# Optimization experiments

Hardware: AMD Instinct MI355X
Metric: run time of the kernel (lower is better)

Reference implementation:

```python
import jax, jax.numpy as jnp
import numpy as np

# Fixed architecture constants (match init_kwargs)
B, CIN, H, W = 2, 3, 224, 224
COUT = 64
KH = KW = 7
SH = SW = 2
PAD = 3
GROUPS = 1
MIX = 4
CG = COUT // GROUPS          # channels per group
REL = CG // 2                # rel_size
PH, PW = H + 2 * PAD, W + 2 * PAD          # padded spatial dims (230, 230)
FH = (PH - KH) // SH + 1                    # output height (112)
FW = (PW - KW) // SW + 1                    # output width  (112)


def setup_inputs() -> dict:
    key = jax.random.key(0)
    ks = jax.random.split(key, 10)
    n = jax.random.normal
    return {
        "x": n(ks[0], (B, CIN, H, W), jnp.float32),
        "weight_query": n(ks[1], (GROUPS, CIN // GROUPS, CG), jnp.float32) * 0.2,
        "weight_key": n(ks[2], (GROUPS, CIN // GROUPS, CG), jnp.float32) * 0.2,
        "weight_value": n(ks[3], (MIX, GROUPS, CIN // GROUPS, CG), jnp.float32) * 0.2,
        "relative_x": n(ks[4], (REL, 1, KW), jnp.float32) * 0.1,
        "relative_y": n(ks[5], (CG - REL, KH, 1), jnp.float32) * 0.1,
        "emb_x": n(ks[6], (CG, 1, PW), jnp.float32) * 0.1,
        "emb_y": n(ks[7], (CG, PH, 1), jnp.float32) * 0.1,
        "emb_m": n(ks[8], (MIX, CG, 1, 1), jnp.float32) * 0.1,
        "bias": n(ks[9], (COUT,), jnp.float32) * 0.05,
    }


def _unfold(t):
    """torch.nn.functional.unfold: (b,c,PH,PW) -> (b,c,KH*KW,FH*FW) with (c,kh,kw) layout."""
    b, c = t.shape[0], t.shape[1]
    ri = jnp.arange(FH) * SH
    rj = jnp.arange(FW) * SW
    p = t[:, :, ri[:, None] + jnp.arange(KH)[None, :], :]          # (b,c,FH,KH,PW)
    p = p[:, :, :, :, rj[:, None] + jnp.arange(KW)[None, :]]       # (b,c,FH,KH,FW,KW)
    return p.transpose(0, 1, 3, 5, 2, 4).reshape(b, c, KH * KW, FH * FW)


def _forward(x, wq, wk, wv, rx, ry, ex, ey, em, bias):
    b = x.shape[0]
    # relative position bias: (COUT, KH*KW, 1)
    rel = jnp.concatenate([jnp.tile(rx, (1, KH, 1)), jnp.tile(ry, (1, 1, KW))], axis=0)
    rel = jnp.tile(rel, (GROUPS, 1, 1)).reshape(COUT, KH * KW, 1)

    xp = jnp.pad(x, ((0, 0), (0, 0), (PAD, PAD), (PAD, PAD)))       # (b,CIN,PH,PW)
    x_ij = xp.transpose(0, 2, 3, 1).reshape(b, PH * PW, GROUPS, CIN // GROUPS)

    # per-pixel grouped projections -> (b, COUT, PH, PW)
    vq = jnp.einsum('bngi,gio->bgon', x_ij, wq).reshape(b, COUT, PH, PW)
    vk = jnp.einsum('bngi,gio->bgon', x_ij, wk).reshape(b, COUT, PH, PW)

    # mixture weights over value transforms: softmax over mix axis, per pixel
    p_ab = ex + ey                                                   # (CG,PH,PW)
    p_abm = jax.nn.softmax(jnp.sum(p_ab[None] * em, axis=1), axis=0) # (MIX,PH,PW)

    vvm = jnp.einsum('bngi,mgio->mbgon', x_ij, wv).reshape(MIX, b, COUT, PH, PW)
    vv = jnp.sum(vvm * p_abm[:, None, None], axis=0)                 # (b,COUT,PH,PW)

    win_k = _unfold(vk)                                              # (b,COUT,KH*KW,L)
    win_v = _unfold(vv)                                              # (b,COUT,KH*KW,L)
    # center query of each window (equivalent to unfold then slice center)
    ci = (KH - 1) // 2 + jnp.arange(FH) * SH
    cj = (KW - 1) // 2 + jnp.arange(FW) * SW
    win_q = vq[:, :, ci[:, None], cj[None, :]].reshape(b, COUT, 1, FH * FW)

    scores = jnp.sum(win_q * (win_k + rel[None]), axis=1)            # (b,KH*KW,L)
    # NOTE: the torch code applies softmax over dim=2 which, after the sum over
    # channels, is the SPATIAL dim (L), not the window dim. Faithful to source.
    attn = jax.nn.softmax(scores, axis=2)                            # (b,KH*KW,L)
    v = jnp.sum(attn[:, None] * win_v, axis=2) + bias[None, :, None] # (b,COUT,L)
    return v.reshape(b, COUT, FH, FW)


def reference(x, weight_query, weight_key, weight_value, relative_x, relative_y, emb_x, emb_y, emb_m, bias):
    return _forward(x, weight_query, weight_key, weight_value, relative_x, relative_y, emb_x, emb_y, emb_m, bias)
```

## Files before the change

### kernel.cpp

```cpp
#include <hip/hip_runtime.h>
#include <math.h>

namespace {
constexpr int Bc = 2, Hc = 224, Wc = 224, HWc = Hc * Wc;
constexpr int COUTc = 64, KHc = 7, KWc = 7, PADc = 3;
constexpr int MIXc = 4, RELc = 32;
constexpr int PHc = 230, PWc = 230;
constexpr int FHc = 112, FWc = 112, NN = FHc * FWc;
constexpr int NK = KHc * KWc;
constexpr int WS_EEX = 0;
constexpr int WS_EEY = WS_EEX + MIXc * PWc;
constexpr int WS_COL = WS_EEY + MIXc * PHc;
constexpr int WS_ACC = 1920;
}

__global__ __launch_bounds__(256) void sam_k0(
    const float* __restrict__ ex, const float* __restrict__ ey,
    const float* __restrict__ em, const float* __restrict__ wq,
    const float* __restrict__ wk, const float* __restrict__ rx,
    const float* __restrict__ ry, float* __restrict__ ws) {
  const int idx = blockIdx.x * 256 + threadIdx.x;
  if (idx < Bc * NK) ws[WS_ACC + idx * 16] = 0.f;

  constexpr int half = MIXc * PWc;
  if (idx < 2 * half) {
    const int which = idx >= half;
    const int r = which ? idx - half : idx;
    const int m = r / PWc, j = r % PWc;
    float s = 0.f;
#pragma unroll 8
    for (int c = 0; c < COUTc; ++c)
      s += (which ? ey[c * PHc + j] : ex[c * PWc + j]) * em[m * COUTc + c];
    ws[idx] = expf(s);
  }

  const int u = idx - 2 * half;
  if (u >= 0 && u < 51) {
    float s = 0.f;
    if (u < 9) {
      const int cj = u / 3, ci = u % 3;
#pragma unroll 8
      for (int o = 0; o < COUTc; ++o) s += wq[cj * COUTc + o] * wk[ci * COUTc + o];
    } else if (u < 30) {
      const int v = u - 9, cj = v / 7, kw = v % 7;
#pragma unroll 8
      for (int o = 0; o < RELc; ++o) s += wq[cj * COUTc + o] * rx[o * KWc + kw];
    } else {
      const int v = u - 30, cj = v / 7, kh = v % 7;
#pragma unroll 8
      for (int o = 0; o < RELc; ++o) s += wq[cj * COUTc + RELc + o] * ry[o * KHc + kh];
    }
    ws[WS_COL + u] = s;
  }
}

__global__ __launch_bounds__(256) void sam_stats(const float* __restrict__ x,
                                                 float* __restrict__ ws) {
  __shared__ float sCol[51];
  const int t = threadIdx.x;
  if (t < 51) sCol[t] = ws[WS_COL + t];
  __syncthreads();

  const int w = t >> 6, lane = t & 63;
  const int k = blockIdx.y * 4 + w;
  if (k >= NK) return;
  const int b = blockIdx.z;
  const int kh = k / 7, kw = k - 7 * kh;
  const int n = blockIdx.x * 64 + lane;
  const int fh = n / FWc, fw = n - fh * FWc;
  const int i0 = 2 * fh, j0 = 2 * fw;
  const float* xb = x + (size_t)b * 3 * HWc;
  const int co = i0 * Wc + j0;
  const float xc0 = xb[co], xc1 = xb[HWc + co], xc2 = xb[2 * HWc + co];
  const float* M = sCol;
  const float* Rx = sCol + 9;
  const float* Ry = sCol + 30;

  float s = xc0 * (Rx[kw] + Ry[kh]) + xc1 * (Rx[7 + kw] + Ry[7 + kh]) +
            xc2 * (Rx[14 + kw] + Ry[14 + kh]);
  const int ir = i0 + kh - PADc, jc = j0 + kw - PADc;
  if ((unsigned)ir < (unsigned)Hc && (unsigned)jc < (unsigned)Wc) {
    const float q0 = xc0 * M[0] + xc1 * M[3] + xc2 * M[6];
    const float q1 = xc0 * M[1] + xc1 * M[4] + xc2 * M[7];
    const float q2 = xc0 * M[2] + xc1 * M[5] + xc2 * M[8];
    const int off = ir * Wc + jc;
    s += q0 * xb[off] + q1 * xb[HWc + off] + q2 * xb[2 * HWc + off];
  }
  float e = expf(s);
#pragma unroll
  for (int m2 = 32; m2; m2 >>= 1) e += __shfl_xor(e, m2, 64);
  if (lane == 0) atomicAdd(ws + WS_ACC + ((size_t)b * NK + k) * 16, e);
}

__global__ __launch_bounds__(512) void sam_out(
    const float* __restrict__ x, const float* __restrict__ wv,
    const float* __restrict__ bias, const float* __restrict__ ws,
    float* __restrict__ out) {
  __shared__ float sCol[51];
  __shared__ float sdninv[NK];
  __shared__ float swv[12 * 64];
  __shared__ float sbias[64];
  __shared__ float sT[8][64][13];

  const int t = threadIdx.x;
  const int b = blockIdx.y;
  if (t < 51) sCol[t] = ws[WS_COL + t];
  if (t < NK) sdninv[t] = 1.f / ws[WS_ACC + ((size_t)b * NK + t) * 16];
  if (t < 64) sbias[t] = bias[t];
  for (int i = t; i < 12 * 64; i += 512) swv[i] = wv[i];
  __syncthreads();

  const int w = t >> 6, l = t & 63;
  const int n = blockIdx.x * 64 + l;
  const int fh = n / FWc, fw = n - fh * FWc;
  const int i0 = 2 * fh, j0 = 2 * fw;
  const float* xb = x + (size_t)b * 3 * HWc;
  const int co = i0 * Wc + j0;
  const float xc0 = xb[co], xc1 = xb[HWc + co], xc2 = xb[2 * HWc + co];
  const float* M = sCol;
  const float* Rx = sCol + 9;
  const float* Ry = sCol + 30;
  const float q0 = xc0 * M[0] + xc1 * M[3] + xc2 * M[6];
  const float q1 = xc0 * M[1] + xc1 * M[4] + xc2 * M[7];
  const float q2 = xc0 * M[2] + xc1 * M[5] + xc2 * M[8];
  float rlx[7], rly[7];
#pragma unroll
  for (int kw = 0; kw < 7; ++kw)
    rlx[kw] = xc0 * Rx[kw] + xc1 * Rx[7 + kw] + xc2 * Rx[14 + kw];
#pragma unroll
  for (int kh = 0; kh < 7; ++kh)
    rly[kh] = xc0 * Ry[kh] + xc1 * Ry[7 + kh] + xc2 * Ry[14 + kh];

  const float* eEX = ws + WS_EEX;
  const float* eEY = ws + WS_EEY;

  float T[12] = {0.f};
#pragma unroll 1
  for (int kk = w; kk < NK; kk += 8) {
    const int kh = kk / 7, kw = kk - 7 * kh;
    const int ir = i0 + kh - PADc, jc = j0 + kw - PADc;
    if ((unsigned)ir >= (unsigned)Hc || (unsigned)jc >= (unsigned)Wc) continue;
    float s = rlx[kw] + rly[kh];
    const int off = ir * Wc + jc;
    const float x0 = xb[off], x1 = xb[HWc + off], x2 = xb[2 * HWc + off];
    s += q0 * x0 + q1 * x1 + q2 * x2;
    const float e = expf(s) * sdninv[kk];
    const int ii = i0 + kh, jj = j0 + kw;
    const float p0 = eEX[jj] * eEY[ii];
    const float p1 = eEX[PWc + jj] * eEY[PHc + ii];
    const float p2 = eEX[2 * PWc + jj] * eEY[2 * PHc + ii];
    const float p3 = eEX[3 * PWc + jj] * eEY[3 * PHc + ii];
    const float wgt = e / (p0 + p1 + p2 + p3);
    const float a0 = wgt * p0, a1 = wgt * p1, a2 = wgt * p2, a3 = wgt * p3;
    T[0] += a0 * x0; T[1]  += a0 * x1; T[2]  += a0 * x2;
    T[3] += a1 * x0; T[4]  += a1 * x1; T[5]  += a1 * x2;
    T[6] += a2 * x0; T[7]  += a2 * x1; T[8]  += a2 * x2;
    T[9] += a3 * x0; T[10] += a3 * x1; T[11] += a3 * x2;
  }
#pragma unroll
  for (int j = 0; j < 12; ++j) sT[w][l][j] = T[j];
  __syncthreads();

  float Tm[12];
#pragma unroll
  for (int j = 0; j < 12; ++j) {
    float s = 0.f;
#pragma unroll
    for (int ww = 0; ww < 8; ++ww) s += sT[ww][l][j];
    Tm[j] = s;
  }
  float* ob = out + (size_t)b * COUTc * NN + n;
#pragma unroll
  for (int oo = 0; oo < 8; ++oo) {
    const int o = w * 8 + oo;
    float acc = sbias[o];
#pragma unroll
    for (int mc = 0; mc < 12; ++mc) acc += swv[mc * 64 + o] * Tm[mc];
    ob[(size_t)o * NN] = acc;
  }
}

extern "C" void kernel_launch(void* const* d_in, const int* in_sizes, int n_in,
                              void* d_out, int out_size, void* d_ws, size_t ws_size,
                              hipStream_t stream) {
  const float* x    = (const float*)d_in[0];
  const float* wq   = (const float*)d_in[1];
  const float* wk   = (const float*)d_in[2];
  const float* wv   = (const float*)d_in[3];
  const float* rx   = (const float*)d_in[4];
  const float* ry   = (const float*)d_in[5];
  const float* ex   = (const float*)d_in[6];
  const float* ey   = (const float*)d_in[7];
  const float* em   = (const float*)d_in[8];
  const float* bias = (const float*)d_in[9];
  float* out = (float*)d_out;
  float* ws  = (float*)d_ws;

  sam_k0<<<dim3(8), 256, 0, stream>>>(ex, ey, em, wq, wk, rx, ry, ws);
  sam_stats<<<dim3(NN / 64, (NK + 3) / 4, Bc), 256, 0, stream>>>(x, ws);
  sam_out<<<dim3(NN / 64, Bc), 512, 0, stream>>>(x, wv, bias, ws, out);
}
```

Before: 102.3 us.

## Replace atomics with partial sums, use fast exp/rcp, retile output kernel

The stats kernel now writes per-block partial sums of exp scores to workspace instead of doing atomicAdd into zeroed slots, so the zeroing in the setup kernel is removed. The output kernel reduces those 196 partials itself before use. Elsewhere expf becomes __expf and the division becomes a hardware reciprocal. The output kernel moves to 256-thread blocks covering 32 pixels each, with a fully unrolled window loop that recomputes the relative terms inline. The fast math intrinsics lower precision, and every output block repeats the partial-sum reduction.

```diff
diff --git a/kernel.cpp b/kernel.cpp
--- a/kernel.cpp
+++ b/kernel.cpp
@@ -8,10 +8,11 @@
 constexpr int PHc = 230, PWc = 230;
 constexpr int FHc = 112, FWc = 112, NN = FHc * FWc;
 constexpr int NK = KHc * KWc;
+constexpr int NCHUNK = 196;
 constexpr int WS_EEX = 0;
 constexpr int WS_EEY = WS_EEX + MIXc * PWc;
 constexpr int WS_COL = WS_EEY + MIXc * PHc;
-constexpr int WS_ACC = 1920;
+constexpr int WS_PART = 1920;
 }
 
 __global__ __launch_bounds__(256) void sam_k0(
@@ -20,8 +21,6 @@
     const float* __restrict__ wk, const float* __restrict__ rx,
     const float* __restrict__ ry, float* __restrict__ ws) {
   const int idx = blockIdx.x * 256 + threadIdx.x;
-  if (idx < Bc * NK) ws[WS_ACC + idx * 16] = 0.f;
-
   constexpr int half = MIXc * PWc;
   if (idx < 2 * half) {
     const int which = idx >= half;
@@ -31,9 +30,8 @@
 #pragma unroll 8
     for (int c = 0; c < COUTc; ++c)
       s += (which ? ey[c * PHc + j] : ex[c * PWc + j]) * em[m * COUTc + c];
-    ws[idx] = expf(s);
-  }
-
+    ws[idx] = __expf(s);
+  }
   const int u = idx - 2 * half;
   if (u >= 0 && u < 51) {
     float s = 0.f;
@@ -72,27 +70,26 @@
   const float* xb = x + (size_t)b * 3 * HWc;
   const int co = i0 * Wc + j0;
   const float xc0 = xb[co], xc1 = xb[HWc + co], xc2 = xb[2 * HWc + co];
-  const float* M = sCol;
-  const float* Rx = sCol + 9;
-  const float* Ry = sCol + 30;
-
-  float s = xc0 * (Rx[kw] + Ry[kh]) + xc1 * (Rx[7 + kw] + Ry[7 + kh]) +
-            xc2 * (Rx[14 + kw] + Ry[14 + kh]);
+
+  float s = xc0 * (sCol[9 + kw] + sCol[30 + kh]) +
+            xc1 * (sCol[16 + kw] + sCol[37 + kh]) +
+            xc2 * (sCol[23 + kw] + sCol[44 + kh]);
   const int ir = i0 + kh - PADc, jc = j0 + kw - PADc;
   if ((unsigned)ir < (unsigned)Hc && (unsigned)jc < (unsigned)Wc) {
-    const float q0 = xc0 * M[0] + xc1 * M[3] + xc2 * M[6];
-    const float q1 = xc0 * M[1] + xc1 * M[4] + xc2 * M[7];
-    const float q2 = xc0 * M[2] + xc1 * M[5] + xc2 * M[8];
+    const float q0 = xc0 * sCol[0] + xc1 * sCol[3] + xc2 * sCol[6];
+    const float q1 = xc0 * sCol[1] + xc1 * sCol[4] + xc2 * sCol[7];
+    const float q2 = xc0 * sCol[2] + xc1 * sCol[5] + xc2 * sCol[8];
     const int off = ir * Wc + jc;
     s += q0 * xb[off] + q1 * xb[HWc + off] + q2 * xb[2 * HWc + off];
   }
-  float e = expf(s);
+  float e = __expf(s);
 #pragma unroll
   for (int m2 = 32; m2; m2 >>= 1) e += __shfl_xor(e, m2, 64);
-  if (lane == 0) atomicAdd(ws + WS_ACC + ((size_t)b * NK + k) * 16, e);
-}
-
-__global__ __launch_bounds__(512) void sam_out(
+  if (lane == 0)
+    ws[WS_PART + ((size_t)b * NK + k) * NCHUNK + blockIdx.x] = e;
+}
+
+__global__ __launch_bounds__(256) void sam_out(
     const float* __restrict__ x, const float* __restrict__ wv,
     const float* __restrict__ bias, const float* __restrict__ ws,
     float* __restrict__ out) {
@@ -100,65 +97,71 @@
   __shared__ float sdninv[NK];
   __shared__ float swv[12 * 64];
   __shared__ float sbias[64];
-  __shared__ float sT[8][64][13];
+  __shared__ float sT[8][32][13];
 
   const int t = threadIdx.x;
   const int b = blockIdx.y;
   if (t < 51) sCol[t] = ws[WS_COL + t];
-  if (t < NK) sdninv[t] = 1.f / ws[WS_ACC + ((size_t)b * NK + t) * 16];
   if (t < 64) sbias[t] = bias[t];
-  for (int i = t; i < 12 * 64; i += 512) swv[i] = wv[i];
+  for (int i = t; i < 12 * 64; i += 256) swv[i] = wv[i];
+  if (t < 4 * NK) {
+    const int k = t >> 2, p = t & 3;
+    const float* base = ws + WS_PART + ((size_t)b * NK + k) * NCHUNK;
+    float s = 0.f;
+    for (int c = p; c < NCHUNK; c += 4) s += base[c];
+    s += __shfl_xor(s, 1, 64);
+    s += __shfl_xor(s, 2, 64);
+    if (p == 0) sdninv[k] = 1.f / s;
+  }
   __syncthreads();
 
-  const int w = t >> 6, l = t & 63;
-  const int n = blockIdx.x * 64 + l;
+  const int g = t >> 5, px = t & 31;
+  const int n = blockIdx.x * 32 + px;
   const int fh = n / FWc, fw = n - fh * FWc;
   const int i0 = 2 * fh, j0 = 2 * fw;
   const float* xb = x + (size_t)b * 3 * HWc;
   const int co = i0 * Wc + j0;
   const float xc0 = xb[co], xc1 = xb[HWc + co], xc2 = xb[2 * HWc + co];
-  const float* M = sCol;
-  const float* Rx = sCol + 9;
-  const float* Ry = sCol + 30;
-  const float q0 = xc0 * M[0] + xc1 * M[3] + xc2 * M[6];
-  const float q1 = xc0 * M[1] + xc1 * M[4] + xc2 * M[7];
-  const float q2 = xc0 * M[2] + xc1 * M[5] + xc2 * M[8];
-  float rlx[7], rly[7];
-#pragma unroll
-  for (int kw = 0; kw < 7; ++kw)
-    rlx[kw] = xc0 * Rx[kw] + xc1 * Rx[7 + kw] + xc2 * Rx[14 + kw];
-#pragma unroll
-  for (int kh = 0; kh < 7; ++kh)
-    rly[kh] = xc0 * Ry[kh] + xc1 * Ry[7 + kh] + xc2 * Ry[14 + kh];
+  const float q0 = xc0 * sCol[0] + xc1 * sCol[3] + xc2 * sCol[6];
+  const float q1 = xc0 * sCol[1] + xc1 * sCol[4] + xc2 * sCol[7];
+  const float q2 = xc0 * sCol[2] + xc1 * sCol[5] + xc2 * sCol[8];
 
   const float* eEX = ws + WS_EEX;
   const float* eEY = ws + WS_EEY;
 
   float T[12] = {0.f};
-#pragma unroll 1
-  for (int kk = w; kk < NK; kk += 8) {
-    const int kh = kk / 7, kw = kk - 7 * kh;
-    const int ir = i0 + kh - PADc, jc = j0 + kw - PADc;
-    if ((unsigned)ir >= (unsigned)Hc || (unsigned)jc >= (unsigned)Wc) continue;
-    float s = rlx[kw] + rly[kh];
-    const int off = ir * Wc + jc;
-    const float x0 = xb[off], x1 = xb[HWc + off], x2 = xb[2 * HWc + off];
-    s += q0 * x0 + q1 * x1 + q2 * x2;
-    const float e = expf(s) * sdninv[kk];
-    const int ii = i0 + kh, jj = j0 + kw;
-    const float p0 = eEX[jj] * eEY[ii];
-    const float p1 = eEX[PWc + jj] * eEY[PHc + ii];
-    const float p2 = eEX[2 * PWc + jj] * eEY[2 * PHc + ii];
-    const float p3 = eEX[3 * PWc + jj] * eEY[3 * PHc + ii];
-    const float wgt = e / (p0 + p1 + p2 + p3);
-    const float a0 = wgt * p0, a1 = wgt * p1, a2 = wgt * p2, a3 = wgt * p3;
-    T[0] += a0 * x0; T[1]  += a0 * x1; T[2]  += a0 * x2;
-    T[3] += a1 * x0; T[4]  += a1 * x1; T[5]  += a1 * x2;
-    T[6] += a2 * x0; T[7]  += a2 * x1; T[8]  += a2 * x2;
-    T[9] += a3 * x0; T[10] += a3 * x1; T[11] += a3 * x2;
-  }
-#pragma unroll
-  for (int j = 0; j < 12; ++j) sT[w][l][j] = T[j];
+#pragma unroll
+  for (int it = 0; it < 7; ++it) {
+    const int kk = g + 8 * it;
+    if (kk < NK) {
+      const int kh = kk / 7, kw = kk - 7 * ((kk * 9363) >> 16);
+      const int kw2 = kk - 7 * kh;
+      (void)kw;
+      const int ir = i0 + kh - PADc, jc = j0 + kw2 - PADc;
+      if ((unsigned)ir < (unsigned)Hc && (unsigned)jc < (unsigned)Wc) {
+        float s = xc0 * (sCol[9 + kw2] + sCol[30 + kh]) +
+                  xc1 * (sCol[16 + kw2] + sCol[37 + kh]) +
+                  xc2 * (sCol[23 + kw2] + sCol[44 + kh]);
+        const int off = ir * Wc + jc;
+        const float x0 = xb[off], x1 = xb[HWc + off], x2 = xb[2 * HWc + off];
+        s += q0 * x0 + q1 * x1 + q2 * x2;
+        const float e = __expf(s) * sdninv[kk];
+        const int ii = i0 + kh, jj = j0 + kw2;
+        const float p0 = eEX[jj] * eEY[ii];
+        const float p1 = eEX[PWc + jj] * eEY[PHc + ii];
+        const float p2 = eEX[2 * PWc + jj] * eEY[2 * PHc + ii];
+        const float p3 = eEX[3 * PWc + jj] * eEY[3 * PHc + ii];
+        const float wgt = e * __builtin_amdgcn_rcpf(p0 + p1 + p2 + p3);
+        const float a0 = wgt * p0, a1 = wgt * p1, a2 = wgt * p2, a3 = wgt * p3;
+        T[0] += a0 * x0; T[1]  += a0 * x1; T[2]  += a0 * x2;
+        T[3] += a1 * x0; T[4]  += a1 * x1; T[5]  += a1 * x2;
+        T[6] += a2 * x0; T[7]  += a2 * x1; T[8]  += a2 * x2;
+        T[9] += a3 * x0; T[10] += a3 * x1; T[11] += a3 * x2;
+      }
+    }
+  }
+#pragma unroll
+  for (int j = 0; j < 12; ++j) sT[g][px][j] = T[j];
   __syncthreads();
 
   float Tm[12];
@@ -166,13 +169,13 @@
   for (int j = 0; j < 12; ++j) {
     float s = 0.f;
 #pragma unroll
-    for (int ww = 0; ww < 8; ++ww) s += sT[ww][l][j];
+    for (int ww = 0; ww < 8; ++ww) s += sT[ww][px][j];
     Tm[j] = s;
   }
   float* ob = out + (size_t)b * COUTc * NN + n;
 #pragma unroll
   for (int oo = 0; oo < 8; ++oo) {
-    const int o = w * 8 + oo;
+    const int o = g * 8 + oo;
     float acc = sbias[o];
 #pragma unroll
     for (int mc = 0; mc < 12; ++mc) acc += swv[mc * 64 + o] * Tm[mc];
@@ -197,6 +200,6 @@
   float* ws  = (float*)d_ws;
 
   sam_k0<<<dim3(8), 256, 0, stream>>>(ex, ey, em, wq, wk, rx, ry, ws);
-  sam_stats<<<dim3(NN / 64, (NK + 3) / 4, Bc), 256, 0, stream>>>(x, ws);
-  sam_out<<<dim3(NN / 64, Bc), 512, 0, stream>>>(x, wv, bias, ws, out);
-}
+  sam_stats<<<dim3(NCHUNK, (NK + 3) / 4, Bc), 256, 0, stream>>>(x, ws);
+  sam_out<<<dim3(NN / 32, Bc), 256, 0, stream>>>(x, wv, bias, ws, out);
+}
```

Measured after the change: 107.4 us. +5.0%, slower.
